# Optimization experiments

Measured on AMD Instinct MI355X. Metric: run time of the kernel, lower is better.

## Reference

```python
import jax, jax.numpy as jnp
import numpy as np

T, B, N, D, HH, H = 32, 2048, 3, 512, 256, 64  # chunk, batch, agents, cent_obs_dim, hypernet hidden, mixer hidden

# rotation indices: row n = [n] + range(0,n) + range(n+1,N)
PERM = jnp.array([[0, 1, 2], [1, 0, 2], [2, 0, 1]])


def _hyper(s, W1, b1, W2, b2):
    # 2-layer hypernet MLP: Linear -> ReLU -> Linear
    return jax.nn.relu(s @ W1 + b1) @ W2 + b2


def setup_inputs() -> dict:
    key = jax.random.key(0)
    ks = jax.random.split(key, 12)

    def p(k, shape, fan_in):
        return jax.random.normal(k, shape, jnp.float32) / np.float32(np.sqrt(fan_in))

    return {
        "agent_q_individual": jax.random.normal(ks[0], (T, B, N), jnp.float32),
        "states": jax.random.normal(ks[1], (T, B, D), jnp.float32),
        # hyper_w1: D -> HH -> N*H
        "hw1_W1": p(ks[2], (D, HH), D), "hw1_b1": jnp.zeros((HH,), jnp.float32),
        "hw1_W2": p(ks[3], (HH, N * H), HH), "hw1_b2": jnp.zeros((N * H,), jnp.float32),
        # hyper_b1: D -> HH -> H
        "hb1_W1": p(ks[4], (D, HH), D), "hb1_b1": jnp.zeros((HH,), jnp.float32),
        "hb1_W2": p(ks[5], (HH, H), HH), "hb1_b2": jnp.zeros((H,), jnp.float32),
        # hyper_w2: D -> HH -> H
        "hw2_W1": p(ks[6], (D, HH), D), "hw2_b1": jnp.zeros((HH,), jnp.float32),
        "hw2_W2": p(ks[7], (HH, H), HH), "hw2_b2": jnp.zeros((H,), jnp.float32),
        # hyper_b2: D -> HH -> 1
        "hb2_W1": p(ks[8], (D, HH), D), "hb2_b1": jnp.zeros((HH,), jnp.float32),
        "hb2_W2": p(ks[9], (HH, 1), HH), "hb2_b2": jnp.zeros((1,), jnp.float32),
    }


def reference(agent_q_individual, states,
              hw1_W1, hw1_b1, hw1_W2, hw1_b2,
              hb1_W1, hb1_b1, hb1_W2, hb1_b2,
              hw2_W1, hw2_b1, hw2_W2, hw2_b2,
              hb2_W1, hb2_b1, hb2_W2, hb2_b2):
    T_, B_ = agent_q_individual.shape[:2]
    s = states  # (T,B,D)

    # Hypernet-generated per-sample mixer weights. The torch .repeat over the
    # agent axis is a pure broadcast here (shared hypernet + same share obs).
    w1 = jnp.abs(_hyper(s, hw1_W1, hw1_b1, hw1_W2, hw1_b2)).reshape(T_, B_, 1, N, H)
    b1 = _hyper(s, hb1_W1, hb1_b1, hb1_W2, hb1_b2).reshape(T_, B_, 1, 1, H)
    w2 = jnp.abs(_hyper(s, hw2_W1, hw2_b1, hw2_W2, hw2_b2)).reshape(T_, B_, 1, H, 1)
    b2 = _hyper(s, hb2_W1, hb2_b1, hb2_W2, hb2_b2).reshape(T_, B_, 1, 1, 1)

    # rotated agent q inputs: (T,B,N,1,N), row n puts q_n first
    q_inps = agent_q_individual[..., PERM][:, :, :, None, :]

    hidden = jax.nn.elu(jnp.matmul(q_inps, w1) + b1)  # (T,B,N,1,H)
    out = jnp.matmul(hidden, w2) + b2                  # (T,B,N,1,1)
    return out.reshape(T_, B_, N)
```

## Files before the change

kernel.cpp:

```cpp
#include <hip/hip_runtime.h>
#include <hip/hip_bf16.h>

typedef __attribute__((ext_vector_type(8))) __bf16 bf16x8;
typedef __attribute__((ext_vector_type(4))) float f32x4;
typedef __attribute__((ext_vector_type(8))) unsigned short ushort8;
typedef unsigned short ushort;

__device__ __forceinline__ ushort f2bf(float f) {
    unsigned u = __builtin_bit_cast(unsigned, f);
    unsigned r = (u + 0x7fffu + ((u >> 16) & 1u)) >> 16;
    return (ushort)r;
}

__device__ __forceinline__ unsigned cvtpk(float a, float b) {
    unsigned r;
    asm("v_cvt_pk_bf16_f32 %0, %1, %2" : "=v"(r) : "v"(a), "v"(b));
    return r;
}

__global__ __launch_bounds__(256) void k_pack(
    const float* __restrict__ w1a, const float* __restrict__ w1b,
    const float* __restrict__ w1c, const float* __restrict__ w1d,
    const float* __restrict__ w2a, const float* __restrict__ w2b,
    const float* __restrict__ w2c, const float* __restrict__ w2d,
    ushort* __restrict__ W1p, ushort* __restrict__ W2p)
{
    int c = blockIdx.x * 256 + threadIdx.x;
    if (c < 65536) {
        int l = c & 63, ks = (c >> 6) & 15, n16 = c >> 10;
        int j = n16 >> 4;
        int col = (n16 & 15) * 16 + (l & 15);
        int kb = ks * 32 + (l >> 4) * 8;
        const float* W = (j == 0) ? w1a : (j == 1) ? w1b : (j == 2) ? w1c : w1d;
        ushort8 o;
#pragma unroll
        for (int e = 0; e < 8; ++e) o[e] = f2bf(W[(size_t)(kb + e) * 256 + col]);
        *reinterpret_cast<ushort8*>(W1p + (size_t)c * 8) = o;
    } else if (c < 65536 + 10752) {
        int cc = c - 65536;
        int l = cc & 63, ks = (cc >> 6) & 7, f = cc >> 9;
        int colg = f * 16 + (l & 15);
        int kb = ks * 32 + (l >> 4) * 8;
        const float* W = nullptr; int lc = 0, ncols = 1;
        if (colg < 192)        { W = w2a; lc = colg;       ncols = 192; }
        else if (colg < 256)   { W = w2b; lc = colg - 192; ncols = 64; }
        else if (colg < 320)   { W = w2c; lc = colg - 256; ncols = 64; }
        else if (colg == 320)  { W = w2d; lc = 0;          ncols = 1; }
        ushort8 o;
#pragma unroll
        for (int e = 0; e < 8; ++e)
            o[e] = W ? f2bf(W[(size_t)(kb + e) * ncols + lc]) : (ushort)0;
        *reinterpret_cast<ushort8*>(W2p + (size_t)cc * 8) = o;
    }
}

__global__ __launch_bounds__(256) void k_l1(
    const float* __restrict__ S, const ushort* __restrict__ W1p,
    const float* __restrict__ b0, const float* __restrict__ b1,
    const float* __restrict__ b2, const float* __restrict__ b3,
    ushort* __restrict__ hid, int m0)
{
    __shared__ ushort sA[64 * 512];
    __shared__ ushort sT[4][64 * 32];
    char* sAb = reinterpret_cast<char*>(sA);

    int tid = threadIdx.x, l = tid & 63, w = tid >> 6;
    int lr = l & 15, lg = l >> 4;
    int mt = blockIdx.x;
    const float* Srow = S + (size_t)(m0 + mt * 64) * 512;

    bf16x8 bbuf[2][8];
    {
        const ushort* base = W1p + (size_t)(w * 16) * 16 * 64 * 8 + (size_t)l * 8;
#pragma unroll
        for (int ks = 0; ks < 2; ++ks)
#pragma unroll
            for (int nf = 0; nf < 4; ++nf)
                bbuf[0][ks * 4 + nf] = *reinterpret_cast<const bf16x8*>(
                    base + ((size_t)nf * 16 + ks) * 64 * 8);
    }

#pragma unroll
    for (int i = 0; i < 16; ++i) {
        int c = i * 256 + tid;
        int row = c >> 6, kc = c & 63;
        const float4* g = reinterpret_cast<const float4*>(Srow + (size_t)row * 512 + kc * 8);
        float4 fa = g[0], fb = g[1];
        uint4 o;
        o.x = cvtpk(fa.x, fa.y); o.y = cvtpk(fa.z, fa.w);
        o.z = cvtpk(fb.x, fb.y); o.w = cvtpk(fb.z, fb.w);
        *reinterpret_cast<uint4*>(sAb + (size_t)(row * 64 + (kc ^ (row & 7))) * 16) = o;
    }
    __syncthreads();

    const float* bp = (w == 0) ? b0 : (w == 1) ? b1 : (w == 2) ? b2 : b3;
    ushort* myT = sT[w];

    for (int cg = 0; cg < 4; ++cg) {
        f32x4 acc[4][4] = {{{0.f}}};
#pragma unroll
        for (int it = 0; it < 8; ++it) {
            {
                int nit = (it + 1) & 7;
                int ncg = (it == 7) ? cg + 1 : cg;
                if (ncg < 4) {
                    const ushort* base = W1p +
                        (((size_t)(w * 16 + ncg * 4) * 16 + (size_t)nit * 2) * 64 + l) * 8;
#pragma unroll
                    for (int ks = 0; ks < 2; ++ks)
#pragma unroll
                        for (int nf = 0; nf < 4; ++nf)
                            bbuf[(it + 1) & 1][ks * 4 + nf] =
                                *reinterpret_cast<const bf16x8*>(
                                    base + ((size_t)nf * 16 * 64 + (size_t)ks * 64) * 8);
                }
            }
            bf16x8 a[2][4];
#pragma unroll
            for (int ks = 0; ks < 2; ++ks)
#pragma unroll
                for (int mf = 0; mf < 4; ++mf) {
                    int row = mf * 16 + lr;
                    int kc = it * 8 + ks * 4 + lg;
                    a[ks][mf] = *reinterpret_cast<const bf16x8*>(
                        sAb + (size_t)(row * 64 + (kc ^ (row & 7))) * 16);
                }
#pragma unroll
            for (int ks = 0; ks < 2; ++ks)
#pragma unroll
                for (int nf = 0; nf < 4; ++nf)
#pragma unroll
                    for (int mf = 0; mf < 4; ++mf)
                        acc[mf][nf] = __builtin_amdgcn_mfma_f32_16x16x32_bf16(
                            a[ks][mf], bbuf[it & 1][ks * 4 + nf], acc[mf][nf], 0, 0, 0);
        }
        int colbase = w * 256 + cg * 64;
        for (int h = 0; h < 2; ++h) {
            asm volatile("s_waitcnt lgkmcnt(0)" ::: "memory");
#pragma unroll
            for (int nf2 = 0; nf2 < 2; ++nf2) {
                int nf = h * 2 + nf2;
                float bv = bp[(colbase + nf * 16 + lr) & 255];
#pragma unroll
                for (int mf = 0; mf < 4; ++mf)
#pragma unroll
                    for (int r = 0; r < 4; ++r) {
                        float v = acc[mf][nf][r] + bv;
                        v = v > 0.f ? v : 0.f;
                        myT[(mf * 16 + lg * 4 + r) * 32 + nf2 * 16 + lr] = f2bf(v);
                    }
            }
            asm volatile("s_waitcnt lgkmcnt(0)" ::: "memory");
#pragma unroll
            for (int i = 0; i < 4; ++i) {
                int idx = i * 64 + l;
                int row = idx >> 2, c8 = idx & 3;
                ushort8 o = *reinterpret_cast<const ushort8*>(myT + row * 32 + c8 * 8);
                *reinterpret_cast<ushort8*>(
                    hid + (size_t)(mt * 64 + row) * 1024 + colbase + h * 32 + c8 * 8) = o;
            }
        }
    }
}

__global__ __launch_bounds__(256) void k_l2mix(
    const ushort* __restrict__ hid, const ushort* __restrict__ W2p,
    const float* __restrict__ bw1, const float* __restrict__ bb1,
    const float* __restrict__ bw2, const float* __restrict__ bb2,
    const float* __restrict__ q, float* __restrict__ out, int m0)
{
    __shared__ float sO[32 * 336];
    int tid = threadIdx.x, l = tid & 63, w = tid >> 6;
    int lr = l & 15, lg = l >> 4;
    int sb = blockIdx.x * 32;

    const int fs[5] = {0, 6, 12, 17, 21};
    int jloaded = -1;
    bf16x8 a[2][8];
    for (int f = fs[w]; f < fs[w + 1]; ++f) {
        int j = (f < 12) ? 0 : (f < 16) ? 1 : (f < 20) ? 2 : 3;
        if (j != jloaded) {
#pragma unroll
            for (int mf = 0; mf < 2; ++mf)
#pragma unroll
                for (int ks = 0; ks < 8; ++ks)
                    a[mf][ks] = *reinterpret_cast<const bf16x8*>(
                        hid + (size_t)(sb + mf * 16 + lr) * 1024 + j * 256 + ks * 32 + lg * 8);
            jloaded = j;
        }
        f32x4 acc[2] = {};
#pragma unroll
        for (int ks = 0; ks < 8; ++ks) {
            bf16x8 b = *reinterpret_cast<const bf16x8*>(W2p + ((size_t)(f * 8 + ks) * 64 + l) * 8);
            acc[0] = __builtin_amdgcn_mfma_f32_16x16x32_bf16(a[0][ks], b, acc[0], 0, 0, 0);
            acc[1] = __builtin_amdgcn_mfma_f32_16x16x32_bf16(a[1][ks], b, acc[1], 0, 0, 0);
        }
        int colg = f * 16 + lr;
        float bv = 0.f; bool doabs = false;
        if (colg < 192)       { bv = bw1[colg];       doabs = true; }
        else if (colg < 256)  { bv = bb1[colg - 192]; doabs = false; }
        else if (colg < 320)  { bv = bw2[colg - 256]; doabs = true; }
        else if (colg == 320) { bv = bb2[0];          doabs = false; }
#pragma unroll
        for (int mf = 0; mf < 2; ++mf)
#pragma unroll
            for (int r = 0; r < 4; ++r) {
                float v = acc[mf][r] + bv;
                if (doabs) v = fabsf(v);
                sO[(mf * 16 + lg * 4 + r) * 336 + colg] = v;
            }
    }
    __syncthreads();

    int sm = tid >> 3, oct = tid & 7;
    const float* qs = q + (size_t)(m0 + sb + sm) * 3;
    float q0 = qs[0], q1 = qs[1], q2 = qs[2];
    const float* ob = sO + sm * 336;
    float res[3];
#pragma unroll
    for (int n = 0; n < 3; ++n) {
        float qa, qb, qc;
        if (n == 0)      { qa = q0; qb = q1; qc = q2; }
        else if (n == 1) { qa = q1; qb = q0; qc = q2; }
        else             { qa = q2; qb = q0; qc = q1; }
        float accm = 0.f;
#pragma unroll
        for (int hh = 0; hh < 8; ++hh) {
            int hc = oct * 8 + hh;
            float hv = ob[192 + hc] + qa * ob[hc] + qb * ob[64 + hc] + qc * ob[128 + hc];
            float ev = hv > 0.f ? hv : expm1f(hv);
            accm += ev * ob[256 + hc];
        }
        accm += __shfl_xor(accm, 1);
        accm += __shfl_xor(accm, 2);
        accm += __shfl_xor(accm, 4);
        res[n] = accm;
    }
    if (oct == 0) {
        float b2v = ob[320];
        float* op = out + (size_t)(m0 + sb + sm) * 3;
        op[0] = res[0] + b2v;
        op[1] = res[1] + b2v;
        op[2] = res[2] + b2v;
    }
}

extern "C" void kernel_launch(void* const* d_in, const int* in_sizes, int n_in,
                              void* d_out, int out_size, void* d_ws, size_t ws_size,
                              hipStream_t stream)
{
    const float* q      = (const float*)d_in[0];
    const float* S      = (const float*)d_in[1];
    const float* hw1_W1 = (const float*)d_in[2];
    const float* hw1_b1 = (const float*)d_in[3];
    const float* hw1_W2 = (const float*)d_in[4];
    const float* hw1_b2 = (const float*)d_in[5];
    const float* hb1_W1 = (const float*)d_in[6];
    const float* hb1_b1 = (const float*)d_in[7];
    const float* hb1_W2 = (const float*)d_in[8];
    const float* hb1_b2 = (const float*)d_in[9];
    const float* hw2_W1 = (const float*)d_in[10];
    const float* hw2_b1 = (const float*)d_in[11];
    const float* hw2_W2 = (const float*)d_in[12];
    const float* hw2_b2 = (const float*)d_in[13];
    const float* hb2_W1 = (const float*)d_in[14];
    const float* hb2_b1 = (const float*)d_in[15];
    const float* hb2_W2 = (const float*)d_in[16];
    const float* hb2_b2 = (const float*)d_in[17];

    int TB = in_sizes[1] / 512;

    ushort* W1p = (ushort*)d_ws;
    ushort* W2p = W1p + (size_t)65536 * 8;
    ushort* hid = W2p + (size_t)10752 * 8;
    size_t used = (size_t)(65536 + 10752) * 16;
    size_t hid_cap = (ws_size > used) ? (ws_size - used) : 0;
    long long max_chunk = (long long)(hid_cap / 2048);
    max_chunk &= ~127LL;
    if (max_chunk > TB) max_chunk = TB;
    if (max_chunk < 128) max_chunk = 128;

    k_pack<<<dim3(298), dim3(256), 0, stream>>>(
        hw1_W1, hb1_W1, hw2_W1, hb2_W1,
        hw1_W2, hb1_W2, hw2_W2, hb2_W2, W1p, W2p);

    for (int m0 = 0; m0 < TB; m0 += (int)max_chunk) {
        int mc = TB - m0;
        if (mc > max_chunk) mc = (int)max_chunk;
        k_l1<<<dim3(mc / 64), dim3(256), 0, stream>>>(
            S, W1p, hw1_b1, hb1_b1, hw2_b1, hb2_b1, hid, m0);
        k_l2mix<<<dim3(mc / 32), dim3(256), 0, stream>>>(
            hid, W2p, hw1_b2, hb1_b2, hw2_b2, hb2_b2, q, (float*)d_out, m0);
    }
}
```

Measured before the change: 170.3 us.

## Deepen W1 prefetch to three-stage ring and narrow epilogue staging tile

Replaces the double-buffered B-fragment prefetch in the layer-1 GEMM with a three-slot register ring that loads two steps ahead, fully unrolls the column-group loop, and inserts a sched_barrier so the global loads are issued before the MFMAs. The epilogue now stages one 16-column fragment at a time through a padded 20-wide LDS tile instead of 32-wide halves, and drops the explicit lgkmcnt waits. The aim is to hide global-load latency for the weights and cut LDS use and bank conflicts. It raises register pressure (24 bf16x8 buffers live), and removing the waits between LDS writes and cross-lane reads depends on the compiler inserting the needed waits for correctness.

```diff
diff --git a/kernel.cpp b/kernel.cpp
--- a/kernel.cpp
+++ b/kernel.cpp
@@ -61,7 +61,7 @@
     ushort* __restrict__ hid, int m0)
 {
     __shared__ ushort sA[64 * 512];
-    __shared__ ushort sT[4][64 * 32];
+    __shared__ ushort sT[4][64 * 20];
     char* sAb = reinterpret_cast<char*>(sA);
 
     int tid = threadIdx.x, l = tid & 63, w = tid >> 6;
@@ -69,16 +69,17 @@
     int mt = blockIdx.x;
     const float* Srow = S + (size_t)(m0 + mt * 64) * 512;
 
-    bf16x8 bbuf[2][8];
-    {
-        const ushort* base = W1p + (size_t)(w * 16) * 16 * 64 * 8 + (size_t)l * 8;
+    const ushort* Wb = W1p + (size_t)w * 131072 + (size_t)l * 8;
+
+    bf16x8 ring[3][8];
+#pragma unroll
+    for (int p = 0; p < 2; ++p)
 #pragma unroll
         for (int ks = 0; ks < 2; ++ks)
 #pragma unroll
             for (int nf = 0; nf < 4; ++nf)
-                bbuf[0][ks * 4 + nf] = *reinterpret_cast<const bf16x8*>(
-                    base + ((size_t)nf * 16 + ks) * 64 * 8);
-    }
+                ring[p][ks * 4 + nf] = *reinterpret_cast<const bf16x8*>(
+                    Wb + nf * 8192 + p * 1024 + ks * 512);
 
 #pragma unroll
     for (int i = 0; i < 16; ++i) {
@@ -96,25 +97,22 @@
     const float* bp = (w == 0) ? b0 : (w == 1) ? b1 : (w == 2) ? b2 : b3;
     ushort* myT = sT[w];
 
+#pragma unroll
     for (int cg = 0; cg < 4; ++cg) {
         f32x4 acc[4][4] = {{{0.f}}};
 #pragma unroll
         for (int it = 0; it < 8; ++it) {
-            {
-                int nit = (it + 1) & 7;
-                int ncg = (it == 7) ? cg + 1 : cg;
-                if (ncg < 4) {
-                    const ushort* base = W1p +
-                        (((size_t)(w * 16 + ncg * 4) * 16 + (size_t)nit * 2) * 64 + l) * 8;
-#pragma unroll
-                    for (int ks = 0; ks < 2; ++ks)
-#pragma unroll
-                        for (int nf = 0; nf < 4; ++nf)
-                            bbuf[(it + 1) & 1][ks * 4 + nf] =
-                                *reinterpret_cast<const bf16x8*>(
-                                    base + ((size_t)nf * 16 * 64 + (size_t)ks * 64) * 8);
-                }
+            const int s = cg * 8 + it;
+            if (s + 2 < 32) {
+                const int s2 = s + 2, cg2 = s2 >> 3, it2 = s2 & 7;
+#pragma unroll
+                for (int ks = 0; ks < 2; ++ks)
+#pragma unroll
+                    for (int nf = 0; nf < 4; ++nf)
+                        ring[s2 % 3][ks * 4 + nf] = *reinterpret_cast<const bf16x8*>(
+                            Wb + cg2 * 32768 + nf * 8192 + it2 * 1024 + ks * 512);
             }
+            __builtin_amdgcn_sched_barrier(0);
             bf16x8 a[2][4];
 #pragma unroll
             for (int ks = 0; ks < 2; ++ks)
@@ -132,32 +130,27 @@
 #pragma unroll
                     for (int mf = 0; mf < 4; ++mf)
                         acc[mf][nf] = __builtin_amdgcn_mfma_f32_16x16x32_bf16(
-                            a[ks][mf], bbuf[it & 1][ks * 4 + nf], acc[mf][nf], 0, 0, 0);
+                            a[ks][mf], ring[s % 3][ks * 4 + nf], acc[mf][nf], 0, 0, 0);
         }
         int colbase = w * 256 + cg * 64;
-        for (int h = 0; h < 2; ++h) {
-            asm volatile("s_waitcnt lgkmcnt(0)" ::: "memory");
-#pragma unroll
-            for (int nf2 = 0; nf2 < 2; ++nf2) {
-                int nf = h * 2 + nf2;
-                float bv = bp[(colbase + nf * 16 + lr) & 255];
-#pragma unroll
-                for (int mf = 0; mf < 4; ++mf)
-#pragma unroll
-                    for (int r = 0; r < 4; ++r) {
-                        float v = acc[mf][nf][r] + bv;
-                        v = v > 0.f ? v : 0.f;
-                        myT[(mf * 16 + lg * 4 + r) * 32 + nf2 * 16 + lr] = f2bf(v);
-                    }
-            }
-            asm volatile("s_waitcnt lgkmcnt(0)" ::: "memory");
-#pragma unroll
-            for (int i = 0; i < 4; ++i) {
+#pragma unroll
+        for (int nf = 0; nf < 4; ++nf) {
+            float bv = bp[(colbase + nf * 16 + lr) & 255];
+#pragma unroll
+            for (int mf = 0; mf < 4; ++mf)
+#pragma unroll
+                for (int r = 0; r < 4; ++r) {
+                    float v = acc[mf][nf][r] + bv;
+                    v = v > 0.f ? v : 0.f;
+                    myT[(mf * 16 + lg * 4 + r) * 20 + lr] = f2bf(v);
+                }
+#pragma unroll
+            for (int i = 0; i < 2; ++i) {
                 int idx = i * 64 + l;
-                int row = idx >> 2, c8 = idx & 3;
-                ushort8 o = *reinterpret_cast<const ushort8*>(myT + row * 32 + c8 * 8);
+                int row = idx >> 1, half = idx & 1;
+                ushort8 o = *reinterpret_cast<const ushort8*>(myT + row * 20 + half * 8);
                 *reinterpret_cast<ushort8*>(
-                    hid + (size_t)(mt * 64 + row) * 1024 + colbase + h * 32 + c8 * 8) = o;
+                    hid + (size_t)(mt * 64 + row) * 1024 + colbase + nf * 16 + half * 8) = o;
             }
         }
     }
```

New measurement: 165.9 us. 1.03x faster.
